# Performance work log

Measured on AMD Instinct MI355X. Metric: run time of the kernel, lower is better.

## Reference

```python
import jax, jax.numpy as jnp
import numpy as np

DURATION = 100.0   # init kwarg: duration
RESOLUTION = 0.1   # init kwarg: resolution
OUT_LEN = int(DURATION / RESOLUTION) + 1  # 1001


def setup_inputs() -> dict:
    key = jax.random.key(0)
    k1, k2 = jax.random.split(key)
    B, S, D = 32, 4096, 256
    embed_batch = jax.random.normal(k1, (B, S, D), dtype=jnp.float32)
    # sorted timestamps spanning [0, DURATION]
    ts_batch = jnp.sort(jax.random.uniform(k2, (B, S), dtype=jnp.float32) * DURATION, axis=-1)
    return {"embed_batch": embed_batch, "ts_batch": ts_batch}


def reference(embed_batch, ts_batch):
    # embed_batch: [B, S, D], ts_batch: [B, S] (sorted along last dim)
    B, S, D = embed_batch.shape
    ts_new = jnp.linspace(0.0, DURATION, OUT_LEN).astype(embed_batch.dtype)  # [L]
    # batched searchsorted replaces the per-sample/per-channel Python loops
    idx = jax.vmap(lambda t: jnp.searchsorted(t, ts_new))(ts_batch)  # [B, L]
    idx = jnp.clip(idx, 1, S - 1)
    lo = idx - 1  # [B, L]
    hi = idx
    x_lo = jnp.take_along_axis(ts_batch, lo, axis=1)  # [B, L]
    x_hi = jnp.take_along_axis(ts_batch, hi, axis=1)
    y_lo = jnp.take_along_axis(embed_batch, lo[:, :, None], axis=1)  # [B, L, D]
    y_hi = jnp.take_along_axis(embed_batch, hi[:, :, None], axis=1)
    slope = (y_hi - y_lo) / (x_hi - x_lo)[:, :, None]
    y_new = slope * (ts_new[None, :, None] - x_lo[:, :, None]) + y_lo
    return y_new  # [B, OUT_LEN, D]
```

## Files before the change

### kernel.cpp

```cpp
#include <hip/hip_runtime.h>


#define RS_B 32
#define RS_S 4096
#define RS_D 256
#define RS_OUTLEN 1001
#define RS_PPW 8
#define RS_NBX ((RS_OUTLEN + RS_PPW - 1) / RS_PPW)
#define RS_NWG (RS_NBX * RS_B)

typedef float f32x4 __attribute__((ext_vector_type(4)));

__global__ __launch_bounds__(64) void resample_kernel(
    const float* __restrict__ embed,
    const float* __restrict__ ts,
    float* __restrict__ out)
{
    const int lin = blockIdx.x;
    const int wg  = (lin & 7) * (RS_NWG / 8) + (lin >> 3);
    const int b   = wg / RS_NBX;
    const int l0  = (wg - b * RS_NBX) * RS_PPW;

    const int lane = threadIdx.x;
    const int p = lane & (RS_PPW - 1);

    int l = l0 + p;
    if (l > RS_OUTLEN - 1) l = RS_OUTLEN - 1;
    const float t = (float)((double)l * (100.0 / 1000.0));

    const float* __restrict__ tsr = ts + (size_t)b * RS_S;

    int lo = 0, hi = RS_S;
#pragma unroll
    for (int it = 0; it < 12; ++it) {
        int mid = (lo + hi) >> 1;
        float v = tsr[mid];
        if (v < t) lo = mid + 1; else hi = mid;
    }
    int idx = lo;
    if (idx < 1) idx = 1;
    if (idx > RS_S - 1) idx = RS_S - 1;

    const float x_lo = tsr[idx - 1];
    const float x_hi = tsr[idx];
    const float w1 = (t - x_lo) / (x_hi - x_lo);

    const f32x4* __restrict__ ebase =
        (const f32x4*)(embed + (size_t)b * RS_S * RS_D);
    f32x4* __restrict__ obase =
        (f32x4*)(out + ((size_t)b * RS_OUTLEN + (size_t)l0) * RS_D);

#pragma unroll
    for (int q = 0; q < RS_PPW; ++q) {
        if (l0 + q > RS_OUTLEN - 1) break;
        const int   sidx = __shfl(idx, q);
        const float sw   = __shfl(w1,  q);

        const f32x4* plo = ebase + (size_t)(sidx - 1) * (RS_D / 4) + lane;
        const f32x4* phi = plo + (RS_D / 4);
        f32x4 a = __builtin_nontemporal_load(plo);
        f32x4 c = __builtin_nontemporal_load(phi);
        f32x4 r = a + (c - a) * sw;
        __builtin_nontemporal_store(r, obase + (size_t)q * (RS_D / 4) + lane);
    }
}

extern "C" void kernel_launch(void* const* d_in, const int* in_sizes, int n_in,
                              void* d_out, int out_size, void* d_ws, size_t ws_size,
                              hipStream_t stream) {
    const float* embed = (const float*)d_in[0];
    const float* ts    = (const float*)d_in[1];
    float* out         = (float*)d_out;

    resample_kernel<<<RS_NWG, 64, 0, stream>>>(embed, ts, out);
}
```

Measured before the change: 22.28 us.

## Replace binary search with two-level ballot search and batch gathers in 4-wave blocks

The 12-step dependent binary search is replaced with a two-level wavefront ballot search. Each lane first reads one coarse pivot every 64 timestamps and popcounts to choose a chunk, then reads that 64-element chunk and popcounts again. All eight output rows of a strip get their indices up front, and their embedding loads are issued together before any stores, to expose memory-level parallelism. Blocks now hold 4 waves (256 threads), and the last strip is clamped so it overlaps and rewrites the tail rows. The cost is extra ts loads per wave and more registers for the staged vectors.

```diff
diff --git a/kernel.cpp b/kernel.cpp
--- a/kernel.cpp
+++ b/kernel.cpp
@@ -6,61 +6,75 @@
 #define RS_D 256
 #define RS_OUTLEN 1001
 #define RS_PPW 8
-#define RS_NBX ((RS_OUTLEN + RS_PPW - 1) / RS_PPW)
-#define RS_NWG (RS_NBX * RS_B)
+#define RS_NSTRIP 126
+#define RS_WPB 4
+#define RS_NBX 32
 
 typedef float f32x4 __attribute__((ext_vector_type(4)));
 
-__global__ __launch_bounds__(64) void resample_kernel(
+__global__ __launch_bounds__(256, 4) void resample_kernel(
     const float* __restrict__ embed,
     const float* __restrict__ ts,
     float* __restrict__ out)
 {
     const int lin = blockIdx.x;
-    const int wg  = (lin & 7) * (RS_NWG / 8) + (lin >> 3);
-    const int b   = wg / RS_NBX;
-    const int l0  = (wg - b * RS_NBX) * RS_PPW;
+    const int wg  = (lin & 7) * (RS_NBX * RS_B / 8) + (lin >> 3);
+    const int b   = wg >> 5;
+    const int bx  = wg & 31;
 
-    const int lane = threadIdx.x;
-    const int p = lane & (RS_PPW - 1);
+    const int wave = threadIdx.x >> 6;
+    const int lane = threadIdx.x & 63;
 
-    int l = l0 + p;
-    if (l > RS_OUTLEN - 1) l = RS_OUTLEN - 1;
-    const float t = (float)((double)l * (100.0 / 1000.0));
+    int sid = bx * RS_WPB + wave;
+    if (sid > RS_NSTRIP - 1) sid = RS_NSTRIP - 1;
+    int l0 = sid * RS_PPW;
+    if (l0 > RS_OUTLEN - RS_PPW) l0 = RS_OUTLEN - RS_PPW;
 
     const float* __restrict__ tsr = ts + (size_t)b * RS_S;
 
-    int lo = 0, hi = RS_S;
+    const float s1 = tsr[lane * 64 + 63];
+    int cq[RS_PPW];
 #pragma unroll
-    for (int it = 0; it < 12; ++it) {
-        int mid = (lo + hi) >> 1;
-        float v = tsr[mid];
-        if (v < t) lo = mid + 1; else hi = mid;
+    for (int q = 0; q < RS_PPW; ++q) {
+        const float tq = (float)((double)(l0 + q) * 0.1);
+        cq[q] = __popcll(__ballot(s1 < tq));
     }
-    int idx = lo;
-    if (idx < 1) idx = 1;
-    if (idx > RS_S - 1) idx = RS_S - 1;
-
-    const float x_lo = tsr[idx - 1];
-    const float x_hi = tsr[idx];
-    const float w1 = (t - x_lo) / (x_hi - x_lo);
+    int idxq[RS_PPW];
+#pragma unroll
+    for (int q = 0; q < RS_PPW; ++q) {
+        const float tq = (float)((double)(l0 + q) * 0.1);
+        const int c = cq[q] < 63 ? cq[q] : 63;
+        const float w = tsr[c * 64 + lane];
+        const int cnt = __popcll(__ballot(w < tq));
+        int idx = (cq[q] >= 64) ? RS_S : c * 64 + cnt;
+        if (idx < 1) idx = 1;
+        if (idx > RS_S - 1) idx = RS_S - 1;
+        idxq[q] = idx;
+    }
+    float swq[RS_PPW];
+#pragma unroll
+    for (int q = 0; q < RS_PPW; ++q) {
+        const float tq = (float)((double)(l0 + q) * 0.1);
+        const float x_lo = tsr[idxq[q] - 1];
+        const float x_hi = tsr[idxq[q]];
+        swq[q] = (tq - x_lo) / (x_hi - x_lo);
+    }
 
     const f32x4* __restrict__ ebase =
         (const f32x4*)(embed + (size_t)b * RS_S * RS_D);
     f32x4* __restrict__ obase =
         (f32x4*)(out + ((size_t)b * RS_OUTLEN + (size_t)l0) * RS_D);
 
+    f32x4 va[RS_PPW], vc[RS_PPW];
 #pragma unroll
     for (int q = 0; q < RS_PPW; ++q) {
-        if (l0 + q > RS_OUTLEN - 1) break;
-        const int   sidx = __shfl(idx, q);
-        const float sw   = __shfl(w1,  q);
-
-        const f32x4* plo = ebase + (size_t)(sidx - 1) * (RS_D / 4) + lane;
-        const f32x4* phi = plo + (RS_D / 4);
-        f32x4 a = __builtin_nontemporal_load(plo);
-        f32x4 c = __builtin_nontemporal_load(phi);
-        f32x4 r = a + (c - a) * sw;
+        const f32x4* plo = ebase + (size_t)(idxq[q] - 1) * (RS_D / 4) + lane;
+        va[q] = __builtin_nontemporal_load(plo);
+        vc[q] = __builtin_nontemporal_load(plo + (RS_D / 4));
+    }
+#pragma unroll
+    for (int q = 0; q < RS_PPW; ++q) {
+        f32x4 r = va[q] + (vc[q] - va[q]) * swq[q];
         __builtin_nontemporal_store(r, obase + (size_t)q * (RS_D / 4) + lane);
     }
 }
@@ -72,5 +86,5 @@
     const float* ts    = (const float*)d_in[1];
     float* out         = (float*)d_out;
 
-    resample_kernel<<<RS_NWG, 64, 0, stream>>>(embed, ts, out);
+    resample_kernel<<<RS_NBX * RS_B, RS_WPB * 64, 0, stream>>>(embed, ts, out);
 }
```

New measurement: 21.09 us, median of 2. -5.3%, faster.

## Split binary search into separate kernel and batch gather loads in payload kernel

Applied to the files above, without the earlier changes.

Moves the per-output binary search over timestamps into its own kernel, which writes interpolation weight and index pairs to workspace. A second kernel with 4 waves per block reads those pairs and issues all 16 embedding row loads before doing any arithmetic, so memory latency overlaps. The aim is to take the dependent search-load chain off the bandwidth-bound gather path. In exchange it adds a second launch and a workspace round trip, and the tail strip is clamped so it overlaps with the previous one and rewrites some rows.

```diff
diff --git a/kernel.cpp b/kernel.cpp
--- a/kernel.cpp
+++ b/kernel.cpp
@@ -6,36 +6,30 @@
 #define RS_D 256
 #define RS_OUTLEN 1001
 #define RS_PPW 8
-#define RS_NBX ((RS_OUTLEN + RS_PPW - 1) / RS_PPW)
-#define RS_NWG (RS_NBX * RS_B)
+#define RS_NSTRIP 126
+#define RS_WPB 4
+#define RS_NBLK (RS_B * RS_NSTRIP / RS_WPB)
+#define RS_WSROW 1008
 
 typedef float f32x4 __attribute__((ext_vector_type(4)));
+typedef float f32x2 __attribute__((ext_vector_type(2)));
 
-__global__ __launch_bounds__(64) void resample_kernel(
-    const float* __restrict__ embed,
+__global__ __launch_bounds__(256) void search_kernel(
     const float* __restrict__ ts,
-    float* __restrict__ out)
+    f32x2* __restrict__ idxw)
 {
-    const int lin = blockIdx.x;
-    const int wg  = (lin & 7) * (RS_NWG / 8) + (lin >> 3);
-    const int b   = wg / RS_NBX;
-    const int l0  = (wg - b * RS_NBX) * RS_PPW;
+    const int b = blockIdx.y;
+    int l = blockIdx.x * 256 + threadIdx.x;
+    if (l > RS_OUTLEN - 1) l = RS_OUTLEN - 1;
 
-    const int lane = threadIdx.x;
-    const int p = lane & (RS_PPW - 1);
-
-    int l = l0 + p;
-    if (l > RS_OUTLEN - 1) l = RS_OUTLEN - 1;
     const float t = (float)((double)l * (100.0 / 1000.0));
-
     const float* __restrict__ tsr = ts + (size_t)b * RS_S;
 
     int lo = 0, hi = RS_S;
 #pragma unroll
     for (int it = 0; it < 12; ++it) {
         int mid = (lo + hi) >> 1;
-        float v = tsr[mid];
-        if (v < t) lo = mid + 1; else hi = mid;
+        if (tsr[mid] < t) lo = mid + 1; else hi = mid;
     }
     int idx = lo;
     if (idx < 1) idx = 1;
@@ -43,24 +37,49 @@
 
     const float x_lo = tsr[idx - 1];
     const float x_hi = tsr[idx];
-    const float w1 = (t - x_lo) / (x_hi - x_lo);
+    f32x2 p;
+    p.x = (t - x_lo) / (x_hi - x_lo);
+    p.y = __int_as_float(idx);
+    idxw[(size_t)b * RS_WSROW + l] = p;
+}
+
+__global__ __launch_bounds__(256, 4) void payload_kernel(
+    const float* __restrict__ embed,
+    const f32x2* __restrict__ idxw,
+    float* __restrict__ out)
+{
+    const int lin = blockIdx.x;
+    const int bkid = (lin & 7) * (RS_NBLK / 8) + (lin >> 3);
+
+    const int wave = threadIdx.x >> 6;
+    const int lane = threadIdx.x & 63;
+
+    const int sid = bkid * RS_WPB + wave;
+    const int b = sid / RS_NSTRIP;
+    int l0 = (sid - b * RS_NSTRIP) * RS_PPW;
+    if (l0 > RS_OUTLEN - RS_PPW) l0 = RS_OUTLEN - RS_PPW;
+
+    const f32x2* __restrict__ prow = idxw + (size_t)b * RS_WSROW + l0;
+    f32x2 pw[RS_PPW];
+#pragma unroll
+    for (int q = 0; q < RS_PPW; ++q) pw[q] = prow[q];
 
     const f32x4* __restrict__ ebase =
         (const f32x4*)(embed + (size_t)b * RS_S * RS_D);
     f32x4* __restrict__ obase =
         (f32x4*)(out + ((size_t)b * RS_OUTLEN + (size_t)l0) * RS_D);
 
+    f32x4 va[RS_PPW], vc[RS_PPW];
 #pragma unroll
     for (int q = 0; q < RS_PPW; ++q) {
-        if (l0 + q > RS_OUTLEN - 1) break;
-        const int   sidx = __shfl(idx, q);
-        const float sw   = __shfl(w1,  q);
-
-        const f32x4* plo = ebase + (size_t)(sidx - 1) * (RS_D / 4) + lane;
-        const f32x4* phi = plo + (RS_D / 4);
-        f32x4 a = __builtin_nontemporal_load(plo);
-        f32x4 c = __builtin_nontemporal_load(phi);
-        f32x4 r = a + (c - a) * sw;
+        const int idx = __float_as_int(pw[q].y);
+        const f32x4* plo = ebase + (size_t)(idx - 1) * (RS_D / 4) + lane;
+        va[q] = __builtin_nontemporal_load(plo);
+        vc[q] = __builtin_nontemporal_load(plo + (RS_D / 4));
+    }
+#pragma unroll
+    for (int q = 0; q < RS_PPW; ++q) {
+        f32x4 r = va[q] + (vc[q] - va[q]) * pw[q].x;
         __builtin_nontemporal_store(r, obase + (size_t)q * (RS_D / 4) + lane);
     }
 }
@@ -71,6 +90,9 @@
     const float* embed = (const float*)d_in[0];
     const float* ts    = (const float*)d_in[1];
     float* out         = (float*)d_out;
+    f32x2* idxw        = (f32x2*)d_ws;
 
-    resample_kernel<<<RS_NWG, 64, 0, stream>>>(embed, ts, out);
+    dim3 g1(4, RS_B);
+    search_kernel<<<g1, 256, 0, stream>>>(ts, idxw);
+    payload_kernel<<<RS_NBLK, RS_WPB * 64, 0, stream>>>(embed, idxw, out);
 }
```

Measured after the change: 25.37 us. +13.8%, slower.
